# Kernel optimization log

Measured on AMD Instinct MI355X. Metric: run time of the kernel, lower is better.

## Reference

```python
import jax, jax.numpy as jnp
import numpy as np

HIDDEN = 2048
NUM_EXPERTS = 64
TOP_K = 2


def setup_inputs() -> dict:
    key = jax.random.key(0)
    k1, k2 = jax.random.split(key)
    x = jax.random.normal(k1, (4, 4096, HIDDEN), dtype=jnp.float32)
    # nn.Linear(hidden, num_experts, bias=False): weight shape [E, H], y = x @ W.T
    W = jax.random.normal(k2, (NUM_EXPERTS, HIDDEN), dtype=jnp.float32) * (HIDDEN ** -0.5)
    return {"x": x, "W": W}


def reference(x, W):
    B, S, H = x.shape
    E, K = NUM_EXPERTS, TOP_K
    xf = x.reshape(-1, H)                       # [N, H]
    gate_logits = xf @ W.T                      # [N, E]
    routing_probs = jax.nn.softmax(gate_logits, axis=-1)
    top_k_probs, top_k_indices = jax.lax.top_k(routing_probs, K)  # [N, K]
    denom = jnp.sum(top_k_probs, axis=-1, keepdims=True) + 1e-6
    routing_weights = (top_k_probs / denom).reshape(B, S, K)
    expert_indices = top_k_indices.reshape(B, S, K)

    # aux load-balancing loss (training path)
    N = xf.shape[0]
    # expert_mask.mean(0): fraction of tokens assigned to each expert
    assign_per_expert = jnp.zeros((E,), jnp.float32).at[top_k_indices.reshape(-1)].add(1.0) / N
    prob_per_expert = jnp.mean(routing_probs, axis=0)             # [E]
    aux_loss = (jnp.sum(prob_per_expert * prob_per_expert) * E
                + jnp.sum(assign_per_expert * assign_per_expert) * E)

    # expert_counts update (bincount over selected indices)
    expert_counts = jnp.zeros((E,), jnp.float32).at[top_k_indices.reshape(-1)].add(1.0)

    return routing_weights, expert_indices, aux_loss, expert_counts
```

## Files before the change

kernel.cpp:

```cpp
#include <hip/hip_runtime.h>

#define HID 2048
#define NEXP 64
#define NTOK 16384
#define TM 32
#define NTHREADS 512
#define NCHUNK 32
#define KPH 8
#define CPW 4
#define TPW 4
#define WS_W_OFF 1024
#define CHUNK_B 24576

#define OUT_IDX_OFF (2 * NTOK)
#define OUT_AUX_OFF (4 * NTOK)
#define OUT_CNT_OFF (4 * NTOK + 1)

typedef __attribute__((ext_vector_type(8))) short bhalf8;
typedef __attribute__((ext_vector_type(16))) float f32x16;

__device__ __forceinline__ void split3(float v, unsigned short& h1, unsigned short& h2, unsigned short& h3) {
    unsigned int u = __float_as_uint(v);
    unsigned int r1 = (u + 0x7FFFu + ((u >> 16) & 1u)) & 0xFFFF0000u;
    float f1 = __uint_as_float(r1);
    float d1 = v - f1;
    unsigned int u2 = __float_as_uint(d1);
    unsigned int r2 = (u2 + 0x7FFFu + ((u2 >> 16) & 1u)) & 0xFFFF0000u;
    float f2 = __uint_as_float(r2);
    float d2 = d1 - f2;
    h1 = (unsigned short)(r1 >> 16);
    h2 = (unsigned short)(r2 >> 16);
    h3 = (unsigned short)(__float_as_uint(d2) >> 16);
}

__device__ __forceinline__ void xsplit(float4 va, float4 vb, bhalf8& o1, bhalf8& o2, bhalf8& o3) {
    float f[8] = {va.x, va.y, va.z, va.w, vb.x, vb.y, vb.z, vb.w};
    union U { bhalf8 v; unsigned int u[4]; } u1, u2, u3;
#pragma unroll
    for (int t = 0; t < 4; t++) {
        float a = f[2 * t], b = f[2 * t + 1];
        unsigned int ua = __float_as_uint(a), ub = __float_as_uint(b);
        float da = a - __uint_as_float(ua & 0xFFFF0000u);
        float db = b - __uint_as_float(ub & 0xFFFF0000u);
        unsigned int uda = __float_as_uint(da), udb = __float_as_uint(db);
        float da2 = da - __uint_as_float(uda & 0xFFFF0000u);
        float db2 = db - __uint_as_float(udb & 0xFFFF0000u);
        u1.u[t] = (ua >> 16) | (ub & 0xFFFF0000u);
        u2.u[t] = (uda >> 16) | (udb & 0xFFFF0000u);
        u3.u[t] = (__float_as_uint(da2) >> 16) | (__float_as_uint(db2) & 0xFFFF0000u);
    }
    o1 = u1.v; o2 = u2.v; o3 = u3.v;
}

__global__ __launch_bounds__(64) void wsplit_kernel(const float* __restrict__ W,
                                                    char* __restrict__ wq,
                                                    float* __restrict__ wsf) {
    if (blockIdx.x < 2) wsf[blockIdx.x * 64 + threadIdx.x] = 0.f;
    int idx8 = (blockIdx.x * 64 + threadIdx.x) * 8;
    int e = idx8 >> 11;
    int k0 = idx8 & 2047;
    int c = k0 >> 6, ks = (k0 >> 4) & 3, half = (k0 >> 3) & 1;
    int g = e >> 5, l = (e & 31) + 32 * half;
    const float4* wp = (const float4*)(W + (size_t)e * HID + k0);
    float4 v0 = wp[0], v1 = wp[1];
    float f[8] = {v0.x, v0.y, v0.z, v0.w, v1.x, v1.y, v1.z, v1.w};
    unsigned int p1[4], p2[4], p3[4];
#pragma unroll
    for (int t = 0; t < 4; t++) {
        unsigned short a1, a2, a3, b1, b2, b3;
        split3(f[2 * t], a1, a2, a3);
        split3(f[2 * t + 1], b1, b2, b3);
        p1[t] = (unsigned int)a1 | ((unsigned int)b1 << 16);
        p2[t] = (unsigned int)a2 | ((unsigned int)b2 << 16);
        p3[t] = (unsigned int)a3 | ((unsigned int)b3 << 16);
    }
    char* base = wq + (size_t)(((c * 4 + ks) * 3 + 0) * 2 + g) * 1024 + l * 16;
    *(uint4*)(base)        = make_uint4(p1[0], p1[1], p1[2], p1[3]);
    *(uint4*)(base + 2048) = make_uint4(p2[0], p2[1], p2[2], p2[3]);
    *(uint4*)(base + 4096) = make_uint4(p3[0], p3[1], p3[2], p3[3]);
}

__global__ __launch_bounds__(NTHREADS, 4) void router_main(
    const float* __restrict__ x, const char* __restrict__ wq,
    float* __restrict__ out, float* __restrict__ ws_accum)
{
    __shared__ float slab[KPH * TM * 68];
    __shared__ float scount[NEXP];
    __shared__ float sprob[NEXP];

    const int tid = threadIdx.x;
    const int w = tid >> 6;
    const int lane = tid & 63;
    const int r = lane & 31;
    const int h = lane >> 5;
    const int n0 = blockIdx.x * TM;

    const float* xrow = x + (size_t)(n0 + r) * HID + h * 8;

    f32x16 acc0, acc1;
#pragma unroll
    for (int i = 0; i < 16; i++) { acc0[i] = 0.f; acc1[i] = 0.f; }

#pragma unroll 1
    for (int i = 0; i < CPW; ++i) {
        const int c = w * CPW + i;
        const float* xc = xrow + c * 64;
        float4 pxa[4], pxb[4];
#pragma unroll
        for (int ks = 0; ks < 4; ks++) {
            pxa[ks] = *(const float4*)(xc + ks * 16);
            pxb[ks] = *(const float4*)(xc + ks * 16 + 4);
        }
        const char* wc = wq + (size_t)c * CHUNK_B + lane * 16;
#pragma unroll
        for (int ks = 0; ks < 4; ks++) {
            bhalf8 A1, A2, A3;
            xsplit(pxa[ks], pxb[ks], A1, A2, A3);
            const char* wk = wc + ks * 6144;
            bhalf8 B1 = *(const bhalf8*)(wk);
            bhalf8 B2 = *(const bhalf8*)(wk + 2048);
            bhalf8 B3 = *(const bhalf8*)(wk + 4096);
            bhalf8 C1 = *(const bhalf8*)(wk + 1024);
            bhalf8 C2 = *(const bhalf8*)(wk + 2048 + 1024);
            bhalf8 C3 = *(const bhalf8*)(wk + 4096 + 1024);
            acc0 = __builtin_amdgcn_mfma_f32_32x32x16_bf16(A1, B1, acc0, 0, 0, 0);
            acc0 = __builtin_amdgcn_mfma_f32_32x32x16_bf16(A1, B2, acc0, 0, 0, 0);
            acc0 = __builtin_amdgcn_mfma_f32_32x32x16_bf16(A2, B1, acc0, 0, 0, 0);
            acc0 = __builtin_amdgcn_mfma_f32_32x32x16_bf16(A1, B3, acc0, 0, 0, 0);
            acc0 = __builtin_amdgcn_mfma_f32_32x32x16_bf16(A2, B2, acc0, 0, 0, 0);
            acc0 = __builtin_amdgcn_mfma_f32_32x32x16_bf16(A3, B1, acc0, 0, 0, 0);
            acc1 = __builtin_amdgcn_mfma_f32_32x32x16_bf16(A1, C1, acc1, 0, 0, 0);
            acc1 = __builtin_amdgcn_mfma_f32_32x32x16_bf16(A1, C2, acc1, 0, 0, 0);
            acc1 = __builtin_amdgcn_mfma_f32_32x32x16_bf16(A2, C1, acc1, 0, 0, 0);
            acc1 = __builtin_amdgcn_mfma_f32_32x32x16_bf16(A1, C3, acc1, 0, 0, 0);
            acc1 = __builtin_amdgcn_mfma_f32_32x32x16_bf16(A2, C2, acc1, 0, 0, 0);
            acc1 = __builtin_amdgcn_mfma_f32_32x32x16_bf16(A3, C1, acc1, 0, 0, 0);
        }
    }

#pragma unroll
    for (int reg = 0; reg < 16; reg++) {
        int row = (reg & 3) + 8 * (reg >> 2) + 4 * h;
        slab[(w * TM + row) * 68 + r]      = acc0[reg];
        slab[(w * TM + row) * 68 + 32 + r] = acc1[reg];
    }
    if (tid < NEXP) { scount[tid] = 0.f; sprob[tid] = 0.f; }
    __syncthreads();

    float* logits = slab;
#pragma unroll
    for (int idx = tid; idx < TM * NEXP; idx += NTHREADS) {
        int t = idx >> 6, e = idx & 63;
        float v = 0.f;
#pragma unroll
        for (int p = 0; p < KPH; p++) v += slab[(p * TM + t) * 68 + e];
        logits[t * 68 + e] = v;
    }
    __syncthreads();

    float pacc = 0.f;
#pragma unroll 1
    for (int j = 0; j < TPW; j++) {
        const int t = w * TPW + j;
        const float v = logits[t * 68 + lane];
        float m1 = v, m2 = -3.4e38f;
        int i1 = lane, i2 = 0;
#pragma unroll
        for (int off = 32; off > 0; off >>= 1) {
            float om1 = __shfl_xor(m1, off);
            int   oi1 = __shfl_xor(i1, off);
            float om2 = __shfl_xor(m2, off);
            int   oi2 = __shfl_xor(i2, off);
            if (om1 > m1 || (om1 == m1 && oi1 < i1)) {
                if (m1 > om2 || (m1 == om2 && i1 < oi2)) { m2 = m1; i2 = i1; }
                else { m2 = om2; i2 = oi2; }
                m1 = om1; i1 = oi1;
            } else {
                if (om1 > m2 || (om1 == m2 && oi1 < i2)) { m2 = om1; i2 = oi1; }
            }
        }
        float p = __expf(v - m1);
        float Z = p;
#pragma unroll
        for (int off = 32; off > 0; off >>= 1) Z += __shfl_xor(Z, off);
        float invZ = 1.f / Z;
        pacc += p * invZ;
        if (lane == 0) {
            float p1 = invZ;
            float p2 = __expf(m2 - m1) * invZ;
            float denom = p1 + p2 + 1e-6f;
            int n = n0 + t;
            out[2 * n + 0] = p1 / denom;
            out[2 * n + 1] = p2 / denom;
            out[OUT_IDX_OFF + 2 * n + 0] = (float)i1;
            out[OUT_IDX_OFF + 2 * n + 1] = (float)i2;
            atomicAdd(&scount[i1], 1.f);
            atomicAdd(&scount[i2], 1.f);
        }
    }
    atomicAdd(&sprob[lane], pacc);
    __syncthreads();

    if (tid < NEXP) {
        atomicAdd(&ws_accum[tid], sprob[tid]);
        atomicAdd(&ws_accum[NEXP + tid], scount[tid]);
    }
}

__global__ void router_finish(const float* __restrict__ ws_accum,
                              float* __restrict__ out)
{
    const int e = threadIdx.x;
    const float invN = 1.f / (float)NTOK;
    float p = ws_accum[e] * invN;
    float a = ws_accum[NEXP + e] * invN;
    float v = p * p + a * a;
#pragma unroll
    for (int off = 32; off > 0; off >>= 1)
        v += __shfl_down(v, off);
    if (e == 0) out[OUT_AUX_OFF] = v * (float)NEXP;
    out[OUT_CNT_OFF + e] = ws_accum[NEXP + e];
}

extern "C" void kernel_launch(void* const* d_in, const int* in_sizes, int n_in,
                              void* d_out, int out_size, void* d_ws, size_t ws_size,
                              hipStream_t stream)
{
    const float* x = (const float*)d_in[0];
    const float* W = (const float*)d_in[1];
    float* out = (float*)d_out;
    float* wsf = (float*)d_ws;
    char* wq = (char*)d_ws + WS_W_OFF;

    wsplit_kernel<<<256, 64, 0, stream>>>(W, wq, wsf);
    router_main<<<NTOK / TM, NTHREADS, 0, stream>>>(x, wq, out, wsf);
    router_finish<<<1, 64, 0, stream>>>(wsf, out);
}
```

Measured before the change: 217.8 us.

## Stage x via global_load_lds double buffering, fuse finish kernel via last-block reduction

Moves x loading to asynchronous global-to-LDS copies with a swizzled, double-buffered layout, so the next half-chunk loads while the current one feeds the MFMAs. Weight fragments are loaded up front per step. The per-wave partial logits are now combined with LDS atomics into a single slab instead of an 8-way slab plus a reduction pass. The separate finish kernel is removed: the last block, found through an atomic counter, computes the aux loss and counts, saving one launch. The costs are a larger LDS footprint (64KB of staging), which lowers occupancy, plus LDS atomic contention and the added complexity of the counter handshake.

```diff
diff --git a/kernel.cpp b/kernel.cpp
--- a/kernel.cpp
+++ b/kernel.cpp
@@ -5,10 +5,10 @@
 #define NTOK 16384
 #define TM 32
 #define NTHREADS 512
-#define NCHUNK 32
 #define KPH 8
 #define CPW 4
 #define TPW 4
+#define NBLK (NTOK / TM)
 #define WS_W_OFF 1024
 #define CHUNK_B 24576
 
@@ -18,6 +18,11 @@
 
 typedef __attribute__((ext_vector_type(8))) short bhalf8;
 typedef __attribute__((ext_vector_type(16))) float f32x16;
+
+__device__ __forceinline__ void stage1k(const void* g, void* l) {
+    __builtin_amdgcn_global_load_lds((const __attribute__((address_space(1))) void*)g,
+                                     (__attribute__((address_space(3))) void*)l, 16, 0, 0);
+}
 
 __device__ __forceinline__ void split3(float v, unsigned short& h1, unsigned short& h2, unsigned short& h3) {
     unsigned int u = __float_as_uint(v);
@@ -55,7 +60,7 @@
 __global__ __launch_bounds__(64) void wsplit_kernel(const float* __restrict__ W,
                                                     char* __restrict__ wq,
                                                     float* __restrict__ wsf) {
-    if (blockIdx.x < 2) wsf[blockIdx.x * 64 + threadIdx.x] = 0.f;
+    if (blockIdx.x < 3) wsf[blockIdx.x * 64 + threadIdx.x] = 0.f;
     int idx8 = (blockIdx.x * 64 + threadIdx.x) * 8;
     int e = idx8 >> 11;
     int k0 = idx8 & 2047;
@@ -82,11 +87,13 @@
 
 __global__ __launch_bounds__(NTHREADS, 4) void router_main(
     const float* __restrict__ x, const char* __restrict__ wq,
-    float* __restrict__ out, float* __restrict__ ws_accum)
+    float* __restrict__ out, float* __restrict__ wsf)
 {
-    __shared__ float slab[KPH * TM * 68];
+    __shared__ __align__(16) char xs[KPH * 8192];
+    __shared__ float slab[TM * 68];
     __shared__ float scount[NEXP];
     __shared__ float sprob[NEXP];
+    __shared__ int slast;
 
     const int tid = threadIdx.x;
     const int w = tid >> 6;
@@ -95,69 +102,85 @@
     const int h = lane >> 5;
     const int n0 = blockIdx.x * TM;
 
-    const float* xrow = x + (size_t)(n0 + r) * HID + h * 8;
+    for (int i = tid; i < TM * 68; i += NTHREADS) slab[i] = 0.f;
+    if (tid < NEXP) { scount[tid] = 0.f; sprob[tid] = 0.f; }
+    __syncthreads();
+
+    const int rl = lane >> 3, sl = lane & 7;
+    const char* gb = (const char*)x + (size_t)(n0 + rl) * (HID * 4) + ((sl * 16) ^ (rl << 4));
+    char* xw = xs + w * 8192;
+    const int swz = (r & 7) << 4;
 
     f32x16 acc0, acc1;
 #pragma unroll
     for (int i = 0; i < 16; i++) { acc0[i] = 0.f; acc1[i] = 0.f; }
 
+    const char* wcb = wq + (size_t)(w * CPW) * CHUNK_B + lane * 16;
+
+    {
+        const char* g0 = gb + (size_t)(w * CPW) * 256;
+#pragma unroll
+        for (int q = 0; q < 4; q++)
+            stage1k(g0 + q * 65536, xw + q * 1024);
+    }
+
 #pragma unroll 1
-    for (int i = 0; i < CPW; ++i) {
-        const int c = w * CPW + i;
-        const float* xc = xrow + c * 64;
-        float4 pxa[4], pxb[4];
-#pragma unroll
-        for (int ks = 0; ks < 4; ks++) {
-            pxa[ks] = *(const float4*)(xc + ks * 16);
-            pxb[ks] = *(const float4*)(xc + ks * 16 + 4);
-        }
-        const char* wc = wq + (size_t)c * CHUNK_B + lane * 16;
-#pragma unroll
-        for (int ks = 0; ks < 4; ks++) {
+    for (int t = 0; t < 2 * CPW; ++t) {
+        const char* wk0 = wcb + (size_t)(t >> 1) * CHUNK_B + (t & 1) * 12288;
+        bhalf8 Bf[2][6];
+#pragma unroll
+        for (int ksl = 0; ksl < 2; ksl++)
+#pragma unroll
+            for (int p5 = 0; p5 < 6; p5++)
+                Bf[ksl][p5] = *(const bhalf8*)(wk0 + ksl * 6144 + p5 * 1024);
+
+        if (t < 2 * CPW - 1) {
+            const int tn = t + 1;
+            const char* gn = gb + (size_t)(w * CPW + (tn >> 1)) * 256 + (tn & 1) * 128;
+            char* ln = xw + (tn & 1) * 4096;
+#pragma unroll
+            for (int q = 0; q < 4; q++)
+                stage1k(gn + q * 65536, ln + q * 1024);
+            __builtin_amdgcn_sched_barrier(0);
+            asm volatile("s_waitcnt vmcnt(4)" ::: "memory");
+            __builtin_amdgcn_sched_barrier(0);
+        } else {
+            __builtin_amdgcn_sched_barrier(0);
+            asm volatile("s_waitcnt vmcnt(0)" ::: "memory");
+            __builtin_amdgcn_sched_barrier(0);
+        }
+
+        const char* xb = xw + (t & 1) * 4096;
+#pragma unroll
+        for (int ksl = 0; ksl < 2; ksl++) {
+            float4 pva = *(const float4*)(xb + r * 128 + ((ksl * 64 + h * 32) ^ swz));
+            float4 pvb = *(const float4*)(xb + r * 128 + ((ksl * 64 + h * 32 + 16) ^ swz));
             bhalf8 A1, A2, A3;
-            xsplit(pxa[ks], pxb[ks], A1, A2, A3);
-            const char* wk = wc + ks * 6144;
-            bhalf8 B1 = *(const bhalf8*)(wk);
-            bhalf8 B2 = *(const bhalf8*)(wk + 2048);
-            bhalf8 B3 = *(const bhalf8*)(wk + 4096);
-            bhalf8 C1 = *(const bhalf8*)(wk + 1024);
-            bhalf8 C2 = *(const bhalf8*)(wk + 2048 + 1024);
-            bhalf8 C3 = *(const bhalf8*)(wk + 4096 + 1024);
-            acc0 = __builtin_amdgcn_mfma_f32_32x32x16_bf16(A1, B1, acc0, 0, 0, 0);
-            acc0 = __builtin_amdgcn_mfma_f32_32x32x16_bf16(A1, B2, acc0, 0, 0, 0);
-            acc0 = __builtin_amdgcn_mfma_f32_32x32x16_bf16(A2, B1, acc0, 0, 0, 0);
-            acc0 = __builtin_amdgcn_mfma_f32_32x32x16_bf16(A1, B3, acc0, 0, 0, 0);
-            acc0 = __builtin_amdgcn_mfma_f32_32x32x16_bf16(A2, B2, acc0, 0, 0, 0);
-            acc0 = __builtin_amdgcn_mfma_f32_32x32x16_bf16(A3, B1, acc0, 0, 0, 0);
-            acc1 = __builtin_amdgcn_mfma_f32_32x32x16_bf16(A1, C1, acc1, 0, 0, 0);
-            acc1 = __builtin_amdgcn_mfma_f32_32x32x16_bf16(A1, C2, acc1, 0, 0, 0);
-            acc1 = __builtin_amdgcn_mfma_f32_32x32x16_bf16(A2, C1, acc1, 0, 0, 0);
-            acc1 = __builtin_amdgcn_mfma_f32_32x32x16_bf16(A1, C3, acc1, 0, 0, 0);
-            acc1 = __builtin_amdgcn_mfma_f32_32x32x16_bf16(A2, C2, acc1, 0, 0, 0);
-            acc1 = __builtin_amdgcn_mfma_f32_32x32x16_bf16(A3, C1, acc1, 0, 0, 0);
+            xsplit(pva, pvb, A1, A2, A3);
+            acc0 = __builtin_amdgcn_mfma_f32_32x32x16_bf16(A1, Bf[ksl][0], acc0, 0, 0, 0);
+            acc0 = __builtin_amdgcn_mfma_f32_32x32x16_bf16(A1, Bf[ksl][2], acc0, 0, 0, 0);
+            acc0 = __builtin_amdgcn_mfma_f32_32x32x16_bf16(A2, Bf[ksl][0], acc0, 0, 0, 0);
+            acc0 = __builtin_amdgcn_mfma_f32_32x32x16_bf16(A1, Bf[ksl][4], acc0, 0, 0, 0);
+            acc0 = __builtin_amdgcn_mfma_f32_32x32x16_bf16(A2, Bf[ksl][2], acc0, 0, 0, 0);
+            acc0 = __builtin_amdgcn_mfma_f32_32x32x16_bf16(A3, Bf[ksl][0], acc0, 0, 0, 0);
+            acc1 = __builtin_amdgcn_mfma_f32_32x32x16_bf16(A1, Bf[ksl][1], acc1, 0, 0, 0);
+            acc1 = __builtin_amdgcn_mfma_f32_32x32x16_bf16(A1, Bf[ksl][3], acc1, 0, 0, 0);
+            acc1 = __builtin_amdgcn_mfma_f32_32x32x16_bf16(A2, Bf[ksl][1], acc1, 0, 0, 0);
+            acc1 = __builtin_amdgcn_mfma_f32_32x32x16_bf16(A1, Bf[ksl][5], acc1, 0, 0, 0);
+            acc1 = __builtin_amdgcn_mfma_f32_32x32x16_bf16(A2, Bf[ksl][3], acc1, 0, 0, 0);
+            acc1 = __builtin_amdgcn_mfma_f32_32x32x16_bf16(A3, Bf[ksl][1], acc1, 0, 0, 0);
         }
     }
 
 #pragma unroll
     for (int reg = 0; reg < 16; reg++) {
         int row = (reg & 3) + 8 * (reg >> 2) + 4 * h;
-        slab[(w * TM + row) * 68 + r]      = acc0[reg];
-        slab[(w * TM + row) * 68 + 32 + r] = acc1[reg];
-    }
-    if (tid < NEXP) { scount[tid] = 0.f; sprob[tid] = 0.f; }
-    __syncthreads();
-
-    float* logits = slab;
-#pragma unroll
-    for (int idx = tid; idx < TM * NEXP; idx += NTHREADS) {
-        int t = idx >> 6, e = idx & 63;
-        float v = 0.f;
-#pragma unroll
-        for (int p = 0; p < KPH; p++) v += slab[(p * TM + t) * 68 + e];
-        logits[t * 68 + e] = v;
-    }
-    __syncthreads();
-
+        atomicAdd(&slab[row * 68 + r],      acc0[reg]);
+        atomicAdd(&slab[row * 68 + 32 + r], acc1[reg]);
+    }
+    __syncthreads();
+
+    const float* logits = slab;
     float pacc = 0.f;
 #pragma unroll 1
     for (int j = 0; j < TPW; j++) {
@@ -202,24 +225,31 @@
     __syncthreads();
 
     if (tid < NEXP) {
-        atomicAdd(&ws_accum[tid], sprob[tid]);
-        atomicAdd(&ws_accum[NEXP + tid], scount[tid]);
-    }
-}
-
-__global__ void router_finish(const float* __restrict__ ws_accum,
-                              float* __restrict__ out)
-{
-    const int e = threadIdx.x;
-    const float invN = 1.f / (float)NTOK;
-    float p = ws_accum[e] * invN;
-    float a = ws_accum[NEXP + e] * invN;
-    float v = p * p + a * a;
-#pragma unroll
-    for (int off = 32; off > 0; off >>= 1)
-        v += __shfl_down(v, off);
-    if (e == 0) out[OUT_AUX_OFF] = v * (float)NEXP;
-    out[OUT_CNT_OFF + e] = ws_accum[NEXP + e];
+        atomicAdd(&wsf[tid], sprob[tid]);
+        atomicAdd(&wsf[NEXP + tid], scount[tid]);
+    }
+
+    __threadfence();
+    if (tid == 0) {
+        unsigned prev = __hip_atomic_fetch_add((unsigned int*)(wsf + 2 * NEXP), 1u,
+                                               __ATOMIC_ACQ_REL, __HIP_MEMORY_SCOPE_AGENT);
+        slast = (prev == NBLK - 1) ? 1 : 0;
+    }
+    __syncthreads();
+    if (slast && tid < NEXP) {
+        const int e = tid;
+        const float invN = 1.f / (float)NTOK;
+        float ps = __hip_atomic_load(wsf + e, __ATOMIC_RELAXED, __HIP_MEMORY_SCOPE_AGENT);
+        float cs = __hip_atomic_load(wsf + NEXP + e, __ATOMIC_RELAXED, __HIP_MEMORY_SCOPE_AGENT);
+        out[OUT_CNT_OFF + e] = cs;
+        float p = ps * invN;
+        float a = cs * invN;
+        float v = p * p + a * a;
+#pragma unroll
+        for (int off = 32; off > 0; off >>= 1)
+            v += __shfl_down(v, off);
+        if (e == 0) out[OUT_AUX_OFF] = v * (float)NEXP;
+    }
 }
 
 extern "C" void kernel_launch(void* const* d_in, const int* in_sizes, int n_in,
@@ -233,6 +263,5 @@
     char* wq = (char*)d_ws + WS_W_OFF;
 
     wsplit_kernel<<<256, 64, 0, stream>>>(W, wq, wsf);
-    router_main<<<NTOK / TM, NTHREADS, 0, stream>>>(x, wq, out, wsf);
-    router_finish<<<1, 64, 0, stream>>>(wsf, out);
-}
+    router_main<<<NBLK, NTHREADS, 0, stream>>>(x, wq, out, wsf);
+}
```

After: 327.0 us. +50.2%, slower.
